# Performance work log

Hardware: AMD Instinct MI355X
Metric: run time of the kernel (lower is better)

## Reference

```python
import jax, jax.numpy as jnp
import numpy as np

VOCAB = 32000
DIM = 128
BATCH = 1024
CONTEXT = 10


def setup_inputs() -> dict:
    key = jax.random.key(0)
    k_idx, k_emb, k_out = jax.random.split(key, 3)
    # context word indices -> one-hot batch [B, C, V], as the original feeds a dense one-hot tensor
    idx = jax.random.randint(k_idx, (BATCH, CONTEXT), 0, VOCAB)
    batch = jax.nn.one_hot(idx, VOCAB, dtype=jnp.float32)
    emb = jax.random.normal(k_emb, (VOCAB, DIM), dtype=jnp.float32)
    w_out = jax.random.normal(k_out, (DIM, VOCAB), dtype=jnp.float32)
    return {"batch": batch, "emb": emb, "w_out": w_out}


def reference(batch, emb, w_out):
    # embedding lookup expressed as one-hot matmul, exactly as the original
    embedding = jnp.einsum('bcv,vd->bcd', batch, emb)      # [B, C, D]
    avg_embedding = jnp.mean(embedding, axis=1)            # [B, D]
    linear_output = avg_embedding @ w_out                  # [B, V]
    return jax.nn.softmax(linear_output, axis=-1)
```

## Files before the change

### kernel.cpp

```cpp
#include <hip/hip_runtime.h>
#include <hip/hip_bf16.h>

#define VOCAB 32000
#define DIM   128
#define BATCH 1024
#define CTX   10
#define SHIFT 20.0f

typedef __bf16 bf16x8 __attribute__((ext_vector_type(8)));
typedef float  f32x4  __attribute__((ext_vector_type(4)));

static __device__ __forceinline__ unsigned short bf16_hi(float x) {
    __hip_bfloat16 h = __float2bfloat16(x);
    return __builtin_bit_cast(unsigned short, h);
}
static __device__ __forceinline__ float bf16_back(unsigned short u) {
    __hip_bfloat16 h = __builtin_bit_cast(__hip_bfloat16, u);
    return __bfloat162float(h);
}


union u4s8 { uint4 v; unsigned short s[8]; };

__global__ __launch_bounds__(256) void convert_w_kernel(
    const float* __restrict__ w, uint4* __restrict__ wsh, uint4* __restrict__ wsl) {
    const int n   = blockIdx.x * 256 + threadIdx.x;
    const int k0i = blockIdx.y;
    const int base = (n >> 4) * 256 + k0i * 64 + (n & 15);
#pragma unroll
    for (int kg = 0; kg < 4; ++kg) {
        u4s8 vh, vl;
#pragma unroll
        for (int j = 0; j < 8; ++j) {
            float x = w[(k0i * 32 + kg * 8 + j) * VOCAB + n];
            unsigned short hh = bf16_hi(x);
            vh.s[j] = hh;
            vl.s[j] = bf16_hi(x - bf16_back(hh));
        }
        wsh[base + kg * 16] = vh.v;
        wsl[base + kg * 16] = vl.v;
    }
}

__global__ __launch_bounds__(256) void onehot_idx_kernel(
    const float* __restrict__ batch, int* __restrict__ idx,
    float* __restrict__ psum) {
    const unsigned int g = blockIdx.x * blockDim.x + threadIdx.x;
    if (g < BATCH) psum[g] = 0.f;

    const unsigned int total4 = (unsigned int)BATCH * CTX * (VOCAB / 4);
    const unsigned int S = gridDim.x * blockDim.x;
    const uint4* __restrict__ b4 = reinterpret_cast<const uint4*>(batch);

    auto emit = [&](uint4 v, unsigned int ii) {
        if ((v.x | v.y | v.z | v.w) != 0u) {
            unsigned int e   = ii * 4u;
            unsigned int row = e / VOCAB;
            unsigned int col = e - row * VOCAB;
            if      (v.x) idx[row] = (int)col;
            else if (v.y) idx[row] = (int)col + 1;
            else if (v.z) idx[row] = (int)col + 2;
            else          idx[row] = (int)col + 3;
        }
    };

    unsigned int i = g;
    for (; i + S < total4; i += 2 * S) {
        uint4 v0 = b4[i];
        uint4 v1 = b4[i + S];
        emit(v0, i);
        emit(v1, i + S);
    }
    if (i < total4) emit(b4[i], i);
}

__global__ __launch_bounds__(128) void avg_emb_kernel(
    const int* __restrict__ idx, const float* __restrict__ emb,
    uint4* __restrict__ ash, uint4* __restrict__ asl) {
    __shared__ unsigned short sh[DIM], sl[DIM];
    const int b = blockIdx.x;
    const int d = threadIdx.x;
    float s = 0.f;
#pragma unroll
    for (int c = 0; c < CTX; ++c) {
        int id = idx[b * CTX + c];
        s += emb[id * DIM + d];
    }
    s *= (1.f / CTX);
    unsigned short hh = bf16_hi(s);
    sh[d] = hh;
    sl[d] = bf16_hi(s - bf16_back(hh));
    __syncthreads();
    if (d < 16) {
        u4s8 vh, vl;
#pragma unroll
        for (int j = 0; j < 8; ++j) { vh.s[j] = sh[d * 8 + j]; vl.s[j] = sl[d * 8 + j]; }
        const int pos = (b >> 4) * 256 + d * 16 + (b & 15);
        ash[pos] = vh.v;
        asl[pos] = vl.v;
    }
}

__global__ __launch_bounds__(256) void gemm_exp_kernel(
    const uint4* __restrict__ ash, const uint4* __restrict__ asl,
    const uint4* __restrict__ wsh, const uint4* __restrict__ wsl,
    float* __restrict__ out, float* __restrict__ psum) {
    const int tid  = threadIdx.x;
    const int wv   = tid >> 6;
    const int lane = tid & 63;
    const int l15  = lane & 15;
    const int kg   = lane >> 4;

    const int m_b0 = blockIdx.y * 128 + wv * 16;
    const int n0   = blockIdx.x * 64;

    f32x4 acc[2][4] = {};

#pragma unroll
    for (int k0i = 0; k0i < 4; ++k0i) {
        bf16x8 a_h[2], a_l[2], b_h[4], b_l[4];
#pragma unroll
        for (int mt = 0; mt < 2; ++mt) {
            const int ai = ((m_b0 + mt * 64) >> 4) * 256 + k0i * 64 + lane;
            a_h[mt] = *reinterpret_cast<const bf16x8*>(ash + ai);
            a_l[mt] = *reinterpret_cast<const bf16x8*>(asl + ai);
        }
#pragma unroll
        for (int nt = 0; nt < 4; ++nt) {
            const int bi = ((n0 >> 4) + nt) * 256 + k0i * 64 + lane;
            b_h[nt] = *reinterpret_cast<const bf16x8*>(wsh + bi);
            b_l[nt] = *reinterpret_cast<const bf16x8*>(wsl + bi);
        }
#pragma unroll
        for (int mt = 0; mt < 2; ++mt)
#pragma unroll
            for (int nt = 0; nt < 4; ++nt) {
                acc[mt][nt] = __builtin_amdgcn_mfma_f32_16x16x32_bf16(a_h[mt], b_h[nt], acc[mt][nt], 0, 0, 0);
                acc[mt][nt] = __builtin_amdgcn_mfma_f32_16x16x32_bf16(a_h[mt], b_l[nt], acc[mt][nt], 0, 0, 0);
                acc[mt][nt] = __builtin_amdgcn_mfma_f32_16x16x32_bf16(a_l[mt], b_h[nt], acc[mt][nt], 0, 0, 0);
            }
    }

#pragma unroll
    for (int mt = 0; mt < 2; ++mt) {
        float rs[4] = {0.f, 0.f, 0.f, 0.f};
#pragma unroll
        for (int nt = 0; nt < 4; ++nt) {
            const int col = n0 + nt * 16 + l15;
#pragma unroll
            for (int r = 0; r < 4; ++r) {
                const int row = m_b0 + mt * 64 + kg * 4 + r;
                float e = __expf(acc[mt][nt][r] - SHIFT);
                out[(long long)row * VOCAB + col] = e;
                rs[r] += e;
            }
        }
#pragma unroll
        for (int r = 0; r < 4; ++r) {
#pragma unroll
            for (int dd = 1; dd < 16; dd <<= 1)
                rs[r] += __shfl_xor(rs[r], dd, 64);
            if (l15 == 0)
                atomicAdd(&psum[m_b0 + mt * 64 + kg * 4 + r], rs[r]);
        }
    }
}

__global__ __launch_bounds__(512) void finalize_kernel(
    const float* __restrict__ psum, float* __restrict__ out) {
    const float inv = 1.f / psum[blockIdx.x];
    float4* p = reinterpret_cast<float4*>(out + (long long)blockIdx.x * VOCAB);
    for (int k = threadIdx.x; k < VOCAB / 4; k += 512) {
        float4 v = p[k];
        v.x *= inv; v.y *= inv; v.z *= inv; v.w *= inv;
        p[k] = v;
    }
}

extern "C" void kernel_launch(void* const* d_in, const int* in_sizes, int n_in,
                              void* d_out, int out_size, void* d_ws, size_t ws_size,
                              hipStream_t stream) {
    const float* batch = (const float*)d_in[0];
    const float* emb   = (const float*)d_in[1];
    const float* w_out = (const float*)d_in[2];
    float*       out   = (float*)d_out;

    char* ws = (char*)d_ws;
    int*   idx  = (int*)ws;   ws += BATCH * CTX * sizeof(int);
    float* psum = (float*)ws; ws += BATCH * sizeof(float);
    ws = (char*)(((size_t)ws + 255) & ~(size_t)255);
    uint4* ash  = (uint4*)ws; ws += (size_t)(BATCH / 16) * 256 * 16;
    uint4* asl  = (uint4*)ws; ws += (size_t)(BATCH / 16) * 256 * 16;
    uint4* wsh  = (uint4*)ws; ws += (size_t)(VOCAB / 16) * 256 * 16;
    uint4* wsl  = (uint4*)ws;

    convert_w_kernel<<<dim3(VOCAB / 256, 4), 256, 0, stream>>>(w_out, wsh, wsl);
    onehot_idx_kernel<<<2048, 256, 0, stream>>>(batch, idx, psum);
    avg_emb_kernel<<<BATCH, DIM, 0, stream>>>(idx, emb, ash, asl);
    gemm_exp_kernel<<<dim3(VOCAB / 64, BATCH / 128), 256, 0, stream>>>(ash, asl, wsh, wsl, out, psum);
    finalize_kernel<<<BATCH, 512, 0, stream>>>(psum, out);
}
```

Baseline: 468.7 us.

## Fuse one-hot scan, embedding average and GEMM into persistent work-queue megakernel

Replaces the separate one-hot scan, embedding-average and GEMM+exp kernels with a persistent kernel that hands out scan items and GEMM tiles through atomic tickets. Once a 128-row slice has all of its averaged embeddings ready, GEMM tiles for that slice can run while other blocks are still scanning the 1.3 GB one-hot input, overlapping compute with the memory-bound scan. The scan now uses nontemporal loads. In exchange it adds spin-waits, atomic ordering that relies on relaxed agent-scope stores being visible, and a fixed grid of 512 blocks whose throughput on the scan phase may differ from the original grid.

After: 745.8 us. 59.1% more time.

```diff
diff --git a/kernel.cpp b/kernel.cpp
--- a/kernel.cpp
+++ b/kernel.cpp
@@ -6,9 +6,15 @@
 #define BATCH 1024
 #define CTX   10
 #define SHIFT 20.0f
+#define NSLICE 8
+#define ROWS_PER_SLICE 128
+#define SCAN_ITEMS (BATCH * 5)
+#define GEMM_X (VOCAB / 64)
+#define MEGA_BLOCKS 512
 
 typedef __bf16 bf16x8 __attribute__((ext_vector_type(8)));
 typedef float  f32x4  __attribute__((ext_vector_type(4)));
+typedef unsigned uintx4 __attribute__((ext_vector_type(4)));
 
 static __device__ __forceinline__ unsigned short bf16_hi(float x) {
     __hip_bfloat16 h = __float2bfloat16(x);
@@ -19,8 +25,40 @@
     return __bfloat162float(h);
 }
 
-
-union u4s8 { uint4 v; unsigned short s[8]; };
+union u4s8 { uint4 v; unsigned short s[8]; unsigned long long q[2]; };
+
+struct Ctl {
+    unsigned scan_ticket;
+    unsigned gemm_ticket[NSLICE];
+    unsigned slice_cnt[NSLICE];
+    unsigned row_cnt[BATCH];
+    int      idx[BATCH * CTX];
+    float    psum[BATCH];
+};
+
+static __device__ __forceinline__ unsigned aadd(unsigned* p, unsigned v) {
+    return __hip_atomic_fetch_add(p, v, __ATOMIC_RELAXED, __HIP_MEMORY_SCOPE_AGENT);
+}
+static __device__ __forceinline__ unsigned aldu(unsigned* p) {
+    return __hip_atomic_load(p, __ATOMIC_RELAXED, __HIP_MEMORY_SCOPE_AGENT);
+}
+static __device__ __forceinline__ int aldi(int* p) {
+    return __hip_atomic_load(p, __ATOMIC_RELAXED, __HIP_MEMORY_SCOPE_AGENT);
+}
+static __device__ __forceinline__ void asti(int* p, int v) {
+    __hip_atomic_store(p, v, __ATOMIC_RELAXED, __HIP_MEMORY_SCOPE_AGENT);
+}
+static __device__ __forceinline__ void astq(unsigned long long* p, unsigned long long v) {
+    __hip_atomic_store(p, v, __ATOMIC_RELAXED, __HIP_MEMORY_SCOPE_AGENT);
+}
+
+__global__ __launch_bounds__(256) void init_kernel(Ctl* c) {
+    const int t = blockIdx.x * 256 + threadIdx.x;
+    if (t == 0) c->scan_ticket = 0;
+    if (t < NSLICE) { c->gemm_ticket[t] = 0; c->slice_cnt[t] = 0; }
+    if (t < BATCH)  { c->row_cnt[t] = 0; c->psum[t] = 0.f; }
+    for (int k = t; k < BATCH * CTX; k += gridDim.x * 256) c->idx[k] = -1;
+}
 
 __global__ __launch_bounds__(256) void convert_w_kernel(
     const float* __restrict__ w, uint4* __restrict__ wsh, uint4* __restrict__ wsl) {
@@ -42,127 +80,172 @@
     }
 }
 
-__global__ __launch_bounds__(256) void onehot_idx_kernel(
-    const float* __restrict__ batch, int* __restrict__ idx,
-    float* __restrict__ psum) {
-    const unsigned int g = blockIdx.x * blockDim.x + threadIdx.x;
-    if (g < BATCH) psum[g] = 0.f;
-
-    const unsigned int total4 = (unsigned int)BATCH * CTX * (VOCAB / 4);
-    const unsigned int S = gridDim.x * blockDim.x;
-    const uint4* __restrict__ b4 = reinterpret_cast<const uint4*>(batch);
-
-    auto emit = [&](uint4 v, unsigned int ii) {
-        if ((v.x | v.y | v.z | v.w) != 0u) {
-            unsigned int e   = ii * 4u;
-            unsigned int row = e / VOCAB;
-            unsigned int col = e - row * VOCAB;
-            if      (v.x) idx[row] = (int)col;
-            else if (v.y) idx[row] = (int)col + 1;
-            else if (v.z) idx[row] = (int)col + 2;
-            else          idx[row] = (int)col + 3;
+__global__ __launch_bounds__(256) void mega_kernel(
+    const float* __restrict__ batch, const float* __restrict__ emb,
+    uint4* __restrict__ ash, uint4* __restrict__ asl,
+    const uint4* __restrict__ wsh, const uint4* __restrict__ wsl,
+    float* __restrict__ out, Ctl* __restrict__ ctl) {
+    const int tid = threadIdx.x;
+
+    __shared__ int s_kind;
+    __shared__ unsigned s_p0, s_p1;
+    __shared__ int s_flag;
+    __shared__ int s_idx[CTX];
+    __shared__ unsigned short s_h[DIM], s_l[DIM];
+
+    unsigned drmask = 0;
+    bool scan_done = false;
+    const bool prefer_gemm = ((blockIdx.x & 3u) == 0u);
+
+    for (;;) {
+        if (tid == 0) {
+            int kind = 3; unsigned p0 = 0, p1 = 0;
+            auto tryScan = [&]() -> bool {
+                if (scan_done) return false;
+                unsigned it = aadd(&ctl->scan_ticket, 1u);
+                if (it >= SCAN_ITEMS) { scan_done = true; return false; }
+                kind = 0; p0 = it; return true;
+            };
+            auto tryGemm = [&]() -> bool {
+                for (unsigned s = 0; s < NSLICE; ++s) {
+                    if (drmask & (1u << s)) continue;
+                    if (aldu(&ctl->slice_cnt[s]) >= ROWS_PER_SLICE) {
+                        unsigned t = aadd(&ctl->gemm_ticket[s], 1u);
+                        if (t < GEMM_X) { kind = 1; p0 = s; p1 = t; return true; }
+                        drmask |= (1u << s);
+                    }
+                }
+                return false;
+            };
+            bool got = prefer_gemm ? (tryGemm() || tryScan())
+                                   : (tryScan() || tryGemm());
+            if (!got && drmask == 0xFFu) kind = 2;
+            s_kind = kind; s_p0 = p0; s_p1 = p1;
         }
-    };
-
-    unsigned int i = g;
-    for (; i + S < total4; i += 2 * S) {
-        uint4 v0 = b4[i];
-        uint4 v1 = b4[i + S];
-        emit(v0, i);
-        emit(v1, i + S);
-    }
-    if (i < total4) emit(b4[i], i);
-}
-
-__global__ __launch_bounds__(128) void avg_emb_kernel(
-    const int* __restrict__ idx, const float* __restrict__ emb,
-    uint4* __restrict__ ash, uint4* __restrict__ asl) {
-    __shared__ unsigned short sh[DIM], sl[DIM];
-    const int b = blockIdx.x;
-    const int d = threadIdx.x;
-    float s = 0.f;
-#pragma unroll
-    for (int c = 0; c < CTX; ++c) {
-        int id = idx[b * CTX + c];
-        s += emb[id * DIM + d];
-    }
-    s *= (1.f / CTX);
-    unsigned short hh = bf16_hi(s);
-    sh[d] = hh;
-    sl[d] = bf16_hi(s - bf16_back(hh));
-    __syncthreads();
-    if (d < 16) {
-        u4s8 vh, vl;
-#pragma unroll
-        for (int j = 0; j < 8; ++j) { vh.s[j] = sh[d * 8 + j]; vl.s[j] = sl[d * 8 + j]; }
-        const int pos = (b >> 4) * 256 + d * 16 + (b & 15);
-        ash[pos] = vh.v;
-        asl[pos] = vl.v;
-    }
-}
-
-__global__ __launch_bounds__(256) void gemm_exp_kernel(
-    const uint4* __restrict__ ash, const uint4* __restrict__ asl,
-    const uint4* __restrict__ wsh, const uint4* __restrict__ wsl,
-    float* __restrict__ out, float* __restrict__ psum) {
-    const int tid  = threadIdx.x;
-    const int wv   = tid >> 6;
-    const int lane = tid & 63;
-    const int l15  = lane & 15;
-    const int kg   = lane >> 4;
-
-    const int m_b0 = blockIdx.y * 128 + wv * 16;
-    const int n0   = blockIdx.x * 64;
-
-    f32x4 acc[2][4] = {};
-
-#pragma unroll
-    for (int k0i = 0; k0i < 4; ++k0i) {
-        bf16x8 a_h[2], a_l[2], b_h[4], b_l[4];
-#pragma unroll
-        for (int mt = 0; mt < 2; ++mt) {
-            const int ai = ((m_b0 + mt * 64) >> 4) * 256 + k0i * 64 + lane;
-            a_h[mt] = *reinterpret_cast<const bf16x8*>(ash + ai);
-            a_l[mt] = *reinterpret_cast<const bf16x8*>(asl + ai);
+        __syncthreads();
+        const int kind = s_kind;
+        const unsigned p0 = s_p0, p1 = s_p1;
+
+        if (kind == 2) break;
+
+        if (kind == 0) {
+            const unsigned b = p0 / 5u, j = p0 - b * 5u;
+            const uintx4* src = reinterpret_cast<const uintx4*>(batch)
+                              + (size_t)(b * CTX + 2 * j) * (VOCAB / 4);
+            int* idxp = ctl->idx + b * CTX + 2 * j;
+
+            auto chk = [&](uintx4 v, int u) {
+                if ((v[0] | v[1] | v[2] | v[3]) != 0u) {
+                    int e = u * 4;
+                    if (!v[0]) e += v[1] ? 1 : (v[2] ? 2 : 3);
+                    int c = (e >= VOCAB) ? 1 : 0;
+                    asti(idxp + c, e - c * VOCAB);
+                }
+            };
+            for (int u = tid; u + 768 < 16000; u += 1024) {
+                uintx4 a0 = __builtin_nontemporal_load(src + u);
+                uintx4 a1 = __builtin_nontemporal_load(src + u + 256);
+                uintx4 a2 = __builtin_nontemporal_load(src + u + 512);
+                uintx4 a3 = __builtin_nontemporal_load(src + u + 768);
+                chk(a0, u); chk(a1, u + 256); chk(a2, u + 512); chk(a3, u + 768);
+            }
+            for (int u = tid + 15360; u < 16000; u += 256)
+                chk(__builtin_nontemporal_load(src + u), u);
+
+            __syncthreads();
+            if (tid == 0) {
+                unsigned old = aadd(&ctl->row_cnt[b], 2u);
+                s_flag = (old == CTX - 2);
+            }
+            __syncthreads();
+            if (s_flag) {
+                if (tid < CTX) {
+                    int v;
+                    do { v = aldi(&ctl->idx[b * CTX + tid]); } while (v < 0);
+                    s_idx[tid] = v;
+                }
+                __syncthreads();
+                if (tid < DIM) {
+                    float s = 0.f;
+#pragma unroll
+                    for (int c = 0; c < CTX; ++c) s += emb[s_idx[c] * DIM + tid];
+                    s *= (1.f / CTX);
+                    unsigned short hh = bf16_hi(s);
+                    s_h[tid] = hh;
+                    s_l[tid] = bf16_hi(s - bf16_back(hh));
+                }
+                __syncthreads();
+                if (tid < 16) {
+                    u4s8 vh, vl;
+#pragma unroll
+                    for (int q = 0; q < 8; ++q) { vh.s[q] = s_h[tid*8+q]; vl.s[q] = s_l[tid*8+q]; }
+                    const int pos = ((int)b >> 4) * 256 + tid * 16 + ((int)b & 15);
+                    unsigned long long* ph = reinterpret_cast<unsigned long long*>(&ash[pos]);
+                    unsigned long long* pl = reinterpret_cast<unsigned long long*>(&asl[pos]);
+                    astq(ph,     vh.q[0]); astq(ph + 1, vh.q[1]);
+                    astq(pl,     vl.q[0]); astq(pl + 1, vl.q[1]);
+                }
+                __syncthreads();
+                if (tid == 0) aadd(&ctl->slice_cnt[b >> 7], 1u);
+            }
+        } else if (kind == 1) {
+            const int wv   = tid >> 6;
+            const int lane = tid & 63;
+            const int l15  = lane & 15;
+            const int kg   = lane >> 4;
+            const int m_b0 = (int)p0 * 128 + wv * 16;
+            const int n0   = (int)p1 * 64;
+
+            f32x4 acc[2][4] = {};
+#pragma unroll
+            for (int k0i = 0; k0i < 4; ++k0i) {
+                bf16x8 a_h[2], a_l[2];
+#pragma unroll
+                for (int mt = 0; mt < 2; ++mt) {
+                    const int ai = ((m_b0 + mt * 64) >> 4) * 256 + k0i * 64 + lane;
+                    a_h[mt] = *reinterpret_cast<const bf16x8*>(ash + ai);
+                    a_l[mt] = *reinterpret_cast<const bf16x8*>(asl + ai);
+                }
+#pragma unroll
+                for (int nt = 0; nt < 4; ++nt) {
+                    const int bi = ((n0 >> 4) + nt) * 256 + k0i * 64 + lane;
+                    bf16x8 b_h = *reinterpret_cast<const bf16x8*>(wsh + bi);
+                    bf16x8 b_l = *reinterpret_cast<const bf16x8*>(wsl + bi);
+#pragma unroll
+                    for (int mt = 0; mt < 2; ++mt) {
+                        acc[mt][nt] = __builtin_amdgcn_mfma_f32_16x16x32_bf16(a_h[mt], b_h, acc[mt][nt], 0, 0, 0);
+                        acc[mt][nt] = __builtin_amdgcn_mfma_f32_16x16x32_bf16(a_h[mt], b_l, acc[mt][nt], 0, 0, 0);
+                        acc[mt][nt] = __builtin_amdgcn_mfma_f32_16x16x32_bf16(a_l[mt], b_h, acc[mt][nt], 0, 0, 0);
+                    }
+                }
+            }
+#pragma unroll
+            for (int mt = 0; mt < 2; ++mt) {
+                float rs[4] = {0.f, 0.f, 0.f, 0.f};
+#pragma unroll
+                for (int nt = 0; nt < 4; ++nt) {
+                    const int col = n0 + nt * 16 + l15;
+#pragma unroll
+                    for (int r = 0; r < 4; ++r) {
+                        const int row = m_b0 + mt * 64 + kg * 4 + r;
+                        float e = __expf(acc[mt][nt][r] - SHIFT);
+                        out[(long long)row * VOCAB + col] = e;
+                        rs[r] += e;
+                    }
+                }
+#pragma unroll
+                for (int r = 0; r < 4; ++r) {
+#pragma unroll
+                    for (int dd = 1; dd < 16; dd <<= 1)
+                        rs[r] += __shfl_xor(rs[r], dd, 64);
+                    if (l15 == 0)
+                        atomicAdd(&ctl->psum[m_b0 + mt * 64 + kg * 4 + r], rs[r]);
+                }
+            }
+        } else {
+            if (tid == 0) __builtin_amdgcn_s_sleep(16);
         }
-#pragma unroll
-        for (int nt = 0; nt < 4; ++nt) {
-            const int bi = ((n0 >> 4) + nt) * 256 + k0i * 64 + lane;
-            b_h[nt] = *reinterpret_cast<const bf16x8*>(wsh + bi);
-            b_l[nt] = *reinterpret_cast<const bf16x8*>(wsl + bi);
-        }
-#pragma unroll
-        for (int mt = 0; mt < 2; ++mt)
-#pragma unroll
-            for (int nt = 0; nt < 4; ++nt) {
-                acc[mt][nt] = __builtin_amdgcn_mfma_f32_16x16x32_bf16(a_h[mt], b_h[nt], acc[mt][nt], 0, 0, 0);
-                acc[mt][nt] = __builtin_amdgcn_mfma_f32_16x16x32_bf16(a_h[mt], b_l[nt], acc[mt][nt], 0, 0, 0);
-                acc[mt][nt] = __builtin_amdgcn_mfma_f32_16x16x32_bf16(a_l[mt], b_h[nt], acc[mt][nt], 0, 0, 0);
-            }
-    }
-
-#pragma unroll
-    for (int mt = 0; mt < 2; ++mt) {
-        float rs[4] = {0.f, 0.f, 0.f, 0.f};
-#pragma unroll
-        for (int nt = 0; nt < 4; ++nt) {
-            const int col = n0 + nt * 16 + l15;
-#pragma unroll
-            for (int r = 0; r < 4; ++r) {
-                const int row = m_b0 + mt * 64 + kg * 4 + r;
-                float e = __expf(acc[mt][nt][r] - SHIFT);
-                out[(long long)row * VOCAB + col] = e;
-                rs[r] += e;
-            }
-        }
-#pragma unroll
-        for (int r = 0; r < 4; ++r) {
-#pragma unroll
-            for (int dd = 1; dd < 16; dd <<= 1)
-                rs[r] += __shfl_xor(rs[r], dd, 64);
-            if (l15 == 0)
-                atomicAdd(&psum[m_b0 + mt * 64 + kg * 4 + r], rs[r]);
-        }
+        __syncthreads();
     }
 }
 
@@ -186,17 +269,15 @@
     float*       out   = (float*)d_out;
 
     char* ws = (char*)d_ws;
-    int*   idx  = (int*)ws;   ws += BATCH * CTX * sizeof(int);
-    float* psum = (float*)ws; ws += BATCH * sizeof(float);
-    ws = (char*)(((size_t)ws + 255) & ~(size_t)255);
-    uint4* ash  = (uint4*)ws; ws += (size_t)(BATCH / 16) * 256 * 16;
-    uint4* asl  = (uint4*)ws; ws += (size_t)(BATCH / 16) * 256 * 16;
-    uint4* wsh  = (uint4*)ws; ws += (size_t)(VOCAB / 16) * 256 * 16;
-    uint4* wsl  = (uint4*)ws;
-
+    Ctl* ctl = (Ctl*)ws;
+    ws += (sizeof(Ctl) + 255) & ~(size_t)255;
+    uint4* ash = (uint4*)ws; ws += (size_t)(BATCH / 16) * 256 * 16;
+    uint4* asl = (uint4*)ws; ws += (size_t)(BATCH / 16) * 256 * 16;
+    uint4* wsh = (uint4*)ws; ws += (size_t)(VOCAB / 16) * 256 * 16;
+    uint4* wsl = (uint4*)ws;
+
+    init_kernel<<<40, 256, 0, stream>>>(ctl);
     convert_w_kernel<<<dim3(VOCAB / 256, 4), 256, 0, stream>>>(w_out, wsh, wsl);
-    onehot_idx_kernel<<<2048, 256, 0, stream>>>(batch, idx, psum);
-    avg_emb_kernel<<<BATCH, DIM, 0, stream>>>(idx, emb, ash, asl);
-    gemm_exp_kernel<<<dim3(VOCAB / 64, BATCH / 128), 256, 0, stream>>>(ash, asl, wsh, wsl, out, psum);
-    finalize_kernel<<<BATCH, 512, 0, stream>>>(psum, out);
-}
+    mega_kernel<<<MEGA_BLOCKS, 256, 0, stream>>>(batch, emb, ash, asl, wsh, wsl, out, ctl);
+    finalize_kernel<<<BATCH, 512, 0, stream>>>(&ctl->psum[0], out);
+}
```
